# Kernel tuning notes

Measured on AMD Instinct MI355X. Metric: run time of the kernel, lower is better.

Reference implementation:

```python
import jax, jax.numpy as jnp
import numpy as np

# Static config (from set_param of the wrapped deformable conv)
N, CIN, H, W = 8, 64, 128, 128
COUT, KH, KW = 64, 3, 3
STRIDE, PAD, DIL = 1, 1, 1
WEIGHT_BIT = 8
K = KH * KW
HO = (H + 2 * PAD - DIL * (KH - 1) - 1) // STRIDE + 1
WO = (W + 2 * PAD - DIL * (KW - 1) - 1) // STRIDE + 1


def setup_inputs() -> dict:
    key = jax.random.key(0)
    k1, k2, k3 = jax.random.split(key, 3)
    x = jax.random.normal(k1, (N, CIN, H, W), dtype=jnp.float32)
    offset = jax.random.normal(k2, (N, 2 * K, HO, WO), dtype=jnp.float32)
    weight = jax.random.normal(k3, (COUT, CIN, KH, KW), dtype=jnp.float32) * 0.05
    return {"x": x, "offset": offset, "weight": weight}


def quantize_weight_symmetric(w, bits):
    # HAWQ/CoDeNet symmetric per-tensor quant: scale = max(|min|,|max|)/n,
    # q = clamp(round(w/scale), -n-1, n) * scale, straight-through estimator.
    n = 2 ** (bits - 1) - 1
    sat = jnp.maximum(jnp.abs(w.min()), jnp.abs(w.max()))
    scale = jnp.maximum(sat, 1e-8) / n
    wq = jnp.clip(jnp.round(w / scale), -n - 1, n) * scale
    return w + jax.lax.stop_gradient(wq - w)


def deform_conv2d(x, offset, weight):
    # x: [N,C,H,W]; offset: [N, 2*K, HO, WO] (y,x interleaved per kernel tap)
    # Base sampling grid for each kernel tap and output location.
    ky, kx = jnp.meshgrid(jnp.arange(KH), jnp.arange(KW), indexing='ij')
    ky = ky.reshape(K).astype(jnp.float32)  # [K]
    kx = kx.reshape(K).astype(jnp.float32)
    ho = jnp.arange(HO, dtype=jnp.float32)
    wo = jnp.arange(WO, dtype=jnp.float32)
    base_y = ho[None, :, None] * STRIDE - PAD + ky[:, None, None] * DIL  # [K,HO,1]
    base_x = wo[None, None, :] * STRIDE - PAD + kx[:, None, None] * DIL  # [K,1,WO]

    off = offset.reshape(N, K, 2, HO, WO)
    py = base_y[None] + off[:, :, 0]  # [N,K,HO,WO]
    px = base_x[None] + off[:, :, 1]

    y0 = jnp.floor(py)
    x0 = jnp.floor(px)
    dy = py - y0
    dx = px - x0
    y0i = y0.astype(jnp.int32)
    x0i = x0.astype(jnp.int32)

    xf = x.reshape(N, CIN, H * W)

    def gather_corner(yi, xi, wgt):
        # zero padding outside the image
        valid = (yi >= 0) & (yi < H) & (xi >= 0) & (xi < W)
        idx = jnp.clip(yi, 0, H - 1) * W + jnp.clip(xi, 0, W - 1)  # [N,K,HO,WO]
        vals = jax.vmap(lambda xn, idn: xn[:, idn.reshape(-1)])(xf, idx)
        vals = vals.reshape(N, CIN, K, HO, WO)
        return vals * (wgt * valid.astype(wgt.dtype))[:, None]  # [N,1,K,HO,WO]

    sampled = (
        gather_corner(y0i, x0i, (1.0 - dy) * (1.0 - dx))
        + gather_corner(y0i, x0i + 1, (1.0 - dy) * dx)
        + gather_corner(y0i + 1, x0i, dy * (1.0 - dx))
        + gather_corner(y0i + 1, x0i + 1, dy * dx)
    )  # [N,CIN,K,HO,WO]

    out = jnp.einsum('nckhw,ock->nohw', sampled, weight.reshape(COUT, CIN, K))
    return out


def reference(x, offset, weight):
    wq = quantize_weight_symmetric(weight, WEIGHT_BIT)
    return deform_conv2d(x, offset, wq)
```

## Files before the change

### kernel.cpp

```cpp
#include <hip/hip_runtime.h>
#include <hip/hip_bf16.h>

#define NB    8
#define CCH   64
#define HH    128
#define WW    128
#define KTAP  9
#define HW    (HH * WW)
#define KSTEPS 18
#define NW    36864

typedef _Float16 f16x8 __attribute__((ext_vector_type(8)));
typedef _Float16 f16x2 __attribute__((ext_vector_type(2)));
typedef __attribute__((ext_vector_type(4))) float f32x4;

__device__ inline unsigned int pack_f16(float a, float b) {
    f16x2 h;
    h[0] = (_Float16)a;
    h[1] = (_Float16)b;
    return __builtin_bit_cast(unsigned int, h);
}

__device__ inline f16x8 as_f16x8(uint4 u) { return __builtin_bit_cast(f16x8, u); }

__global__ __launch_bounds__(256) void prep_kernel(const float* __restrict__ x,
                                                   const float* __restrict__ w,
                                                   unsigned int* __restrict__ xt32,
                                                   uint4* __restrict__ bq) {
    __shared__ float tile[64 * 65];
    const int t = threadIdx.x;
    const int bid = blockIdx.x;

    if (bid < 2048) {
        const int n = bid >> 8;
        const int pbase = (bid & 255) * 64;
        #pragma unroll
        for (int i = 0; i < 4; i++) {
            int idx = i * 256 + t;
            int c = idx >> 4, f4 = idx & 15;
            float4 v = *(const float4*)&x[((size_t)(n * CCH + c)) * HW + pbase + f4 * 4];
            float* d = &tile[c * 65 + f4 * 4];
            d[0] = v.x; d[1] = v.y; d[2] = v.z; d[3] = v.w;
        }
        __syncthreads();
        const int px = t >> 2, c4 = t & 3;
        float f[16];
        #pragma unroll
        for (int j = 0; j < 16; j++) f[j] = tile[(c4 * 16 + j) * 65 + px];
        unsigned int o8[8];
        #pragma unroll
        for (int i = 0; i < 8; i++) o8[i] = pack_f16(f[2 * i], f[2 * i + 1]);
        uint4* dst = (uint4*)&xt32[((size_t)(n * HW + pbase + px)) * 32 + c4 * 8];
        dst[0] = make_uint4(o8[0], o8[1], o8[2], o8[3]);
        dst[1] = make_uint4(o8[4], o8[5], o8[6], o8[7]);
    } else {
        float m0 = 0.f, m1 = 0.f, m2 = 0.f, m3 = 0.f;
        for (int i = t; i < NW; i += 1024) {
            m0 = fmaxf(m0, fabsf(w[i]));
            m1 = fmaxf(m1, fabsf(w[i + 256]));
            m2 = fmaxf(m2, fabsf(w[i + 512]));
            m3 = fmaxf(m3, fabsf(w[i + 768]));
        }
        float m = fmaxf(fmaxf(m0, m1), fmaxf(m2, m3));
        #pragma unroll
        for (int off = 32; off > 0; off >>= 1)
            m = fmaxf(m, __shfl_down(m, off));
        if ((t & 63) == 0) tile[t >> 6] = m;
        __syncthreads();
        m = fmaxf(fmaxf(tile[0], tile[1]), fmaxf(tile[2], tile[3]));
        const float scale = fmaxf(m, 1e-8f) / 127.f;
        const float inv_scale = 1.f / scale;

        const int rec = (bid - 2048) * 256 + t;
        int nt  = rec / (KSTEPS * 64);
        int rem = rec - nt * (KSTEPS * 64);
        int s    = rem >> 6;
        int lane = rem & 63;
        int quad = lane >> 4, n16 = lane & 15;
        int o = nt * 16 + n16;
        unsigned int u[4];
        #pragma unroll
        for (int jj = 0; jj < 4; jj++) {
            float q[2];
            #pragma unroll
            for (int h = 0; h < 2; h++) {
                int k   = s * 32 + quad * 8 + 2 * jj + h;
                int c   = k & 63;
                int tap = k >> 6;
                float v  = w[(o * CCH + c) * KTAP + tap];
                float qq = rintf(v * inv_scale);
                q[h] = fminf(fmaxf(qq, -128.f), 127.f) * scale;
            }
            u[jj] = pack_f16(q[0], q[1]);
        }
        bq[rec] = make_uint4(u[0], u[1], u[2], u[3]);
    }
}

__global__ __launch_bounds__(256) void deform_mfma(const unsigned short* __restrict__ xt,
                                                   const float* __restrict__ offset,
                                                   const uint4* __restrict__ bq,
                                                   float* __restrict__ out) {
    __shared__ unsigned int SC[576];
    __shared__ uint2 SW[576];
    __shared__ _Float16 Abuf[2][64 * 64];

    const int t    = threadIdx.x;
    const int wid  = t >> 6;
    const int lane = t & 63;
    const int quad = lane >> 4, n16 = lane & 15;
    const int bid  = blockIdx.x;
    const int n    = bid & 7;
    const int px0  = (bid >> 3) * 64;
    const int pl   = t >> 2;
    const int c4   = t & 3;

    const char* xb = (const char*)(xt + (size_t)n * HW * CCH);
    const float* offn = offset + (size_t)n * 2 * KTAP * HW;
    const uint4* bqw = bq + (size_t)wid * KSTEPS * 64 + lane;

    for (int u = t; u < 576; u += 256) {
        const int tap = u >> 6, p = u & 63;
        const int ppx = px0 + p;
        const int ho = ppx >> 7, wo = ppx & 127;
        const int ky = tap / 3, kx = tap - 3 * ky;
        const float py  = (float)(ho - 1 + ky) + offn[(2 * tap) * HW + ppx];
        const float pxf = (float)(wo - 1 + kx) + offn[(2 * tap + 1) * HW + ppx];
        const float fy = floorf(py), fx = floorf(pxf);
        const int y0 = (int)fy, x0 = (int)fx;
        const float dy = py - fy, dx = pxf - fx;
        const int y1 = y0 + 1, x1 = x0 + 1;
        const bool vy0 = (y0 >= 0) && (y0 < HH);
        const bool vy1 = (y1 >= 0) && (y1 < HH);
        const bool vx0 = (x0 >= 0) && (x0 < WW);
        const bool vx1 = (x1 >= 0) && (x1 < WW);
        const int y0c = min(max(y0, 0), HH - 1);
        const int y1c = min(max(y1, 0), HH - 1);
        const int x0c = min(max(x0, 0), WW - 1);
        const int x1c = min(max(x1, 0), WW - 1);
        const float w00 = (1.f - dy) * (1.f - dx) * ((vy0 && vx0) ? 1.f : 0.f);
        const float w01 = (1.f - dy) * dx         * ((vy0 && vx1) ? 1.f : 0.f);
        const float w10 = dy * (1.f - dx)         * ((vy1 && vx0) ? 1.f : 0.f);
        const float w11 = dy * dx                 * ((vy1 && vx1) ? 1.f : 0.f);
        SC[u] = (unsigned)(y0c | (x0c << 7) | (y1c << 14) | (x1c << 21));
        SW[u] = make_uint2(pack_f16(w00, w01), pack_f16(w10, w11));
    }

    f32x4 acc[4];
    #pragma unroll
    for (int mt = 0; mt < 4; mt++) acc[mt] = (f32x4){0.f, 0.f, 0.f, 0.f};

    const int cb = c4 * 16;
    const int p7 = pl & 7;

    uint4 rbuf[2][8];
    uint4 bbuf[2][2];

    auto issue = [&](int tap, int b) {
        bbuf[b][0] = bqw[(tap * 2 + 0) * 64];
        bbuf[b][1] = bqw[(tap * 2 + 1) * 64];
        const unsigned int cc = SC[tap * 64 + pl];
        const int y0b = (int)(cc & 127) << 14;
        const int x0b = (int)((cc >> 7) & 127) << 7;
        const int y1b = (int)((cc >> 14) & 127) << 14;
        const int x1b = (int)(cc >> 21) << 7;
        const char* q00 = xb + (y0b | x0b) + cb;
        const char* q01 = xb + (y0b | x1b) + cb;
        const char* q10 = xb + (y1b | x0b) + cb;
        const char* q11 = xb + (y1b | x1b) + cb;
        rbuf[b][0] = *(const uint4*)q00; rbuf[b][1] = *(const uint4*)(q00 + 64);
        rbuf[b][2] = *(const uint4*)q01; rbuf[b][3] = *(const uint4*)(q01 + 64);
        rbuf[b][4] = *(const uint4*)q10; rbuf[b][5] = *(const uint4*)(q10 + 64);
        rbuf[b][6] = *(const uint4*)q11; rbuf[b][7] = *(const uint4*)(q11 + 64);
    };

    auto blend = [&](int tap, int b) {
        const uint2 ww = SW[tap * 64 + pl];
        const f16x2 wA = __builtin_bit_cast(f16x2, ww.x);
        const f16x2 wB = __builtin_bit_cast(f16x2, ww.y);
        f16x8 sa = as_f16x8(rbuf[b][0]) * wA[0];
        sa += as_f16x8(rbuf[b][2]) * wA[1];
        sa += as_f16x8(rbuf[b][4]) * wB[0];
        sa += as_f16x8(rbuf[b][6]) * wB[1];
        f16x8 sb = as_f16x8(rbuf[b][1]) * wA[0];
        sb += as_f16x8(rbuf[b][3]) * wA[1];
        sb += as_f16x8(rbuf[b][5]) * wB[0];
        sb += as_f16x8(rbuf[b][7]) * wB[1];
        *(f16x8*)&Abuf[b][pl * 64 + ((c4 ^ p7) * 8)]       = sa;
        *(f16x8*)&Abuf[b][pl * 64 + (((4 + c4) ^ p7) * 8)] = sb;
    };

    auto mma_tap = [&](int tap, int b) {
        #pragma unroll
        for (int sl = 0; sl < 2; sl++) {
            const f16x8 bf = __builtin_bit_cast(f16x8, bbuf[b][sl]);
            #pragma unroll
            for (int mt = 0; mt < 4; mt++) {
                const int rr = mt * 16 + n16;
                const int slot = (sl * 4 + quad) ^ (n16 & 7);
                const f16x8 a = *(const f16x8*)&Abuf[b][rr * 64 + slot * 8];
                acc[mt] = __builtin_amdgcn_mfma_f32_16x16x32_f16(a, bf, acc[mt], 0, 0, 0);
            }
        }
    };

    __syncthreads();
    issue(0, 0);
    #pragma unroll
    for (int tap = 0; tap < KTAP; tap++) {
        if (tap < KTAP - 1) issue(tap + 1, (tap + 1) & 1);
        blend(tap, tap & 1);
        __syncthreads();
        mma_tap(tap, tap & 1);
    }

    const int o = wid * 16 + n16;
    #pragma unroll
    for (int mt = 0; mt < 4; mt++) {
        float4 v = make_float4(acc[mt].x, acc[mt].y, acc[mt].z, acc[mt].w);
        float* dst = out + ((size_t)(n * CCH + o)) * HW + px0 + mt * 16 + quad * 4;
        *(float4*)dst = v;
    }
}

extern "C" void kernel_launch(void* const* d_in, const int* in_sizes, int n_in,
                              void* d_out, int out_size, void* d_ws, size_t ws_size,
                              hipStream_t stream) {
    const float* x      = (const float*)d_in[0];
    const float* offset = (const float*)d_in[1];
    const float* weight = (const float*)d_in[2];
    float* out = (float*)d_out;

    unsigned char* ws = (unsigned char*)d_ws;
    uint4*        bq   = (uint4*)ws;
    unsigned int* xt32 = (unsigned int*)(ws + 131072);
    const unsigned short* xt = (const unsigned short*)xt32;

    prep_kernel<<<2048 + 18, 256, 0, stream>>>(x, weight, xt32, bq);
    deform_mfma<<<2048, 256, 0, stream>>>(xt, offset, bq, out);
}
```

Before: 132.2 us.

## Feed blended samples straight into MFMA registers, dropping LDS staging and double buffering

Each wave now owns 16 pixels and computes the bilinear blend directly in the MFMA A-operand register layout, then loops over all four output-channel tiles. This removes the shared-memory A buffer, its write/read traffic and the per-tap block barriers. In exchange it drops the software prefetch of the next tap (the loop is now unroll 1), and each wave reloads the full weight set for all channel tiles, which raises global/L2 weight traffic and may expose gather latency.

```diff
diff --git a/kernel.cpp b/kernel.cpp
--- a/kernel.cpp
+++ b/kernel.cpp
@@ -103,7 +103,6 @@
                                                    float* __restrict__ out) {
     __shared__ unsigned int SC[576];
     __shared__ uint2 SW[576];
-    __shared__ _Float16 Abuf[2][64 * 64];
 
     const int t    = threadIdx.x;
     const int wid  = t >> 6;
@@ -112,12 +111,10 @@
     const int bid  = blockIdx.x;
     const int n    = bid & 7;
     const int px0  = (bid >> 3) * 64;
-    const int pl   = t >> 2;
-    const int c4   = t & 3;
+    const int mypix = wid * 16 + n16;
 
     const char* xb = (const char*)(xt + (size_t)n * HW * CCH);
     const float* offn = offset + (size_t)n * 2 * KTAP * HW;
-    const uint4* bqw = bq + (size_t)wid * KSTEPS * 64 + lane;
 
     for (int u = t; u < 576; u += 256) {
         const int tap = u >> 6, p = u & 63;
@@ -145,21 +142,17 @@
         SC[u] = (unsigned)(y0c | (x0c << 7) | (y1c << 14) | (x1c << 21));
         SW[u] = make_uint2(pack_f16(w00, w01), pack_f16(w10, w11));
     }
+    __syncthreads();
 
     f32x4 acc[4];
     #pragma unroll
-    for (int mt = 0; mt < 4; mt++) acc[mt] = (f32x4){0.f, 0.f, 0.f, 0.f};
-
-    const int cb = c4 * 16;
-    const int p7 = pl & 7;
-
-    uint4 rbuf[2][8];
-    uint4 bbuf[2][2];
-
-    auto issue = [&](int tap, int b) {
-        bbuf[b][0] = bqw[(tap * 2 + 0) * 64];
-        bbuf[b][1] = bqw[(tap * 2 + 1) * 64];
-        const unsigned int cc = SC[tap * 64 + pl];
+    for (int nt = 0; nt < 4; nt++) acc[nt] = (f32x4){0.f, 0.f, 0.f, 0.f};
+
+    const int cb = quad * 16;
+
+    #pragma unroll 1
+    for (int tap = 0; tap < KTAP; tap++) {
+        const unsigned int cc = SC[tap * 64 + mypix];
         const int y0b = (int)(cc & 127) << 14;
         const int x0b = (int)((cc >> 7) & 127) << 7;
         const int y1b = (int)((cc >> 14) & 127) << 14;
@@ -168,57 +161,44 @@
         const char* q01 = xb + (y0b | x1b) + cb;
         const char* q10 = xb + (y1b | x0b) + cb;
         const char* q11 = xb + (y1b | x1b) + cb;
-        rbuf[b][0] = *(const uint4*)q00; rbuf[b][1] = *(const uint4*)(q00 + 64);
-        rbuf[b][2] = *(const uint4*)q01; rbuf[b][3] = *(const uint4*)(q01 + 64);
-        rbuf[b][4] = *(const uint4*)q10; rbuf[b][5] = *(const uint4*)(q10 + 64);
-        rbuf[b][6] = *(const uint4*)q11; rbuf[b][7] = *(const uint4*)(q11 + 64);
-    };
-
-    auto blend = [&](int tap, int b) {
-        const uint2 ww = SW[tap * 64 + pl];
+        uint4 r0 = *(const uint4*)q00, r1 = *(const uint4*)(q00 + 64);
+        uint4 r2 = *(const uint4*)q01, r3 = *(const uint4*)(q01 + 64);
+        uint4 r4 = *(const uint4*)q10, r5 = *(const uint4*)(q10 + 64);
+        uint4 r6 = *(const uint4*)q11, r7 = *(const uint4*)(q11 + 64);
+
+        uint4 bf[8];
+        #pragma unroll
+        for (int nt = 0; nt < 4; nt++) {
+            bf[nt * 2 + 0] = bq[((nt * KSTEPS) + tap * 2 + 0) * 64 + lane];
+            bf[nt * 2 + 1] = bq[((nt * KSTEPS) + tap * 2 + 1) * 64 + lane];
+        }
+
+        const uint2 ww = SW[tap * 64 + mypix];
         const f16x2 wA = __builtin_bit_cast(f16x2, ww.x);
         const f16x2 wB = __builtin_bit_cast(f16x2, ww.y);
-        f16x8 sa = as_f16x8(rbuf[b][0]) * wA[0];
-        sa += as_f16x8(rbuf[b][2]) * wA[1];
-        sa += as_f16x8(rbuf[b][4]) * wB[0];
-        sa += as_f16x8(rbuf[b][6]) * wB[1];
-        f16x8 sb = as_f16x8(rbuf[b][1]) * wA[0];
-        sb += as_f16x8(rbuf[b][3]) * wA[1];
-        sb += as_f16x8(rbuf[b][5]) * wB[0];
-        sb += as_f16x8(rbuf[b][7]) * wB[1];
-        *(f16x8*)&Abuf[b][pl * 64 + ((c4 ^ p7) * 8)]       = sa;
-        *(f16x8*)&Abuf[b][pl * 64 + (((4 + c4) ^ p7) * 8)] = sb;
-    };
-
-    auto mma_tap = [&](int tap, int b) {
-        #pragma unroll
-        for (int sl = 0; sl < 2; sl++) {
-            const f16x8 bf = __builtin_bit_cast(f16x8, bbuf[b][sl]);
-            #pragma unroll
-            for (int mt = 0; mt < 4; mt++) {
-                const int rr = mt * 16 + n16;
-                const int slot = (sl * 4 + quad) ^ (n16 & 7);
-                const f16x8 a = *(const f16x8*)&Abuf[b][rr * 64 + slot * 8];
-                acc[mt] = __builtin_amdgcn_mfma_f32_16x16x32_f16(a, bf, acc[mt], 0, 0, 0);
-            }
-        }
-    };
-
-    __syncthreads();
-    issue(0, 0);
+        f16x8 sa = as_f16x8(r0) * wA[0];
+        sa += as_f16x8(r2) * wA[1];
+        sa += as_f16x8(r4) * wB[0];
+        sa += as_f16x8(r6) * wB[1];
+        f16x8 sb = as_f16x8(r1) * wA[0];
+        sb += as_f16x8(r3) * wA[1];
+        sb += as_f16x8(r5) * wB[0];
+        sb += as_f16x8(r7) * wB[1];
+
+        #pragma unroll
+        for (int nt = 0; nt < 4; nt++) {
+            acc[nt] = __builtin_amdgcn_mfma_f32_16x16x32_f16(
+                sa, __builtin_bit_cast(f16x8, bf[nt * 2 + 0]), acc[nt], 0, 0, 0);
+            acc[nt] = __builtin_amdgcn_mfma_f32_16x16x32_f16(
+                sb, __builtin_bit_cast(f16x8, bf[nt * 2 + 1]), acc[nt], 0, 0, 0);
+        }
+    }
+
     #pragma unroll
-    for (int tap = 0; tap < KTAP; tap++) {
-        if (tap < KTAP - 1) issue(tap + 1, (tap + 1) & 1);
-        blend(tap, tap & 1);
-        __syncthreads();
-        mma_tap(tap, tap & 1);
-    }
-
-    const int o = wid * 16 + n16;
-    #pragma unroll
-    for (int mt = 0; mt < 4; mt++) {
-        float4 v = make_float4(acc[mt].x, acc[mt].y, acc[mt].z, acc[mt].w);
-        float* dst = out + ((size_t)(n * CCH + o)) * HW + px0 + mt * 16 + quad * 4;
+    for (int nt = 0; nt < 4; nt++) {
+        const int o = nt * 16 + n16;
+        float4 v = make_float4(acc[nt].x, acc[nt].y, acc[nt].z, acc[nt].w);
+        float* dst = out + ((size_t)(n * CCH + o)) * HW + px0 + wid * 16 + quad * 4;
         *(float4*)dst = v;
     }
 }
```

New measurement: 179.5 us. 35.8% more time.

## Process two taps per pipeline stage to halve block barriers

Applied to the files above, without the earlier changes.

Restructures the main loop so each stage gathers, blends and multiplies two kernel taps at once, cutting the stage count from nine to five and the number of __syncthreads barriers accordingly. The shared A buffer grows to hold two taps per stage, doubling LDS use. Gathers for the next stage are now issued after the current blend instead of before it, so less gather latency is hidden behind the blend. The larger per-stage register set may lower occupancy.

```diff
diff --git a/kernel.cpp b/kernel.cpp
--- a/kernel.cpp
+++ b/kernel.cpp
@@ -101,9 +101,9 @@
                                                    const float* __restrict__ offset,
                                                    const uint4* __restrict__ bq,
                                                    float* __restrict__ out) {
+    __shared__ _Float16 Abuf[2][2][4096];
     __shared__ unsigned int SC[576];
     __shared__ uint2 SW[576];
-    __shared__ _Float16 Abuf[2][64 * 64];
 
     const int t    = threadIdx.x;
     const int wid  = t >> 6;
@@ -114,10 +114,11 @@
     const int px0  = (bid >> 3) * 64;
     const int pl   = t >> 2;
     const int c4   = t & 3;
+    const int cb   = c4 * 16;
+    const int p7   = pl & 7;
 
     const char* xb = (const char*)(xt + (size_t)n * HW * CCH);
     const float* offn = offset + (size_t)n * 2 * KTAP * HW;
-    const uint4* bqw = bq + (size_t)wid * KSTEPS * 64 + lane;
 
     for (int u = t; u < 576; u += 256) {
         const int tap = u >> 6, p = u & 63;
@@ -145,20 +146,16 @@
         SC[u] = (unsigned)(y0c | (x0c << 7) | (y1c << 14) | (x1c << 21));
         SW[u] = make_uint2(pack_f16(w00, w01), pack_f16(w10, w11));
     }
+    __syncthreads();
 
     f32x4 acc[4];
     #pragma unroll
     for (int mt = 0; mt < 4; mt++) acc[mt] = (f32x4){0.f, 0.f, 0.f, 0.f};
 
-    const int cb = c4 * 16;
-    const int p7 = pl & 7;
-
-    uint4 rbuf[2][8];
-    uint4 bbuf[2][2];
-
-    auto issue = [&](int tap, int b) {
-        bbuf[b][0] = bqw[(tap * 2 + 0) * 64];
-        bbuf[b][1] = bqw[(tap * 2 + 1) * 64];
+    uint4 rset[16];
+    uint4 bset[2][4];
+
+    auto gather8 = [&](int tap, uint4* r) {
         const unsigned int cc = SC[tap * 64 + pl];
         const int y0b = (int)(cc & 127) << 14;
         const int x0b = (int)((cc >> 7) & 127) << 7;
@@ -168,50 +165,59 @@
         const char* q01 = xb + (y0b | x1b) + cb;
         const char* q10 = xb + (y1b | x0b) + cb;
         const char* q11 = xb + (y1b | x1b) + cb;
-        rbuf[b][0] = *(const uint4*)q00; rbuf[b][1] = *(const uint4*)(q00 + 64);
-        rbuf[b][2] = *(const uint4*)q01; rbuf[b][3] = *(const uint4*)(q01 + 64);
-        rbuf[b][4] = *(const uint4*)q10; rbuf[b][5] = *(const uint4*)(q10 + 64);
-        rbuf[b][6] = *(const uint4*)q11; rbuf[b][7] = *(const uint4*)(q11 + 64);
-    };
-
-    auto blend = [&](int tap, int b) {
+        r[0] = *(const uint4*)q00; r[1] = *(const uint4*)(q00 + 64);
+        r[2] = *(const uint4*)q01; r[3] = *(const uint4*)(q01 + 64);
+        r[4] = *(const uint4*)q10; r[5] = *(const uint4*)(q10 + 64);
+        r[6] = *(const uint4*)q11; r[7] = *(const uint4*)(q11 + 64);
+    };
+    auto issue_stage = [&](int s) {
+        gather8(2 * s, rset);
+        if (s < 4) gather8(2 * s + 1, rset + 8);
+        const int nk = (s < 4) ? 4 : 2;
+        for (int k = 0; k < nk; k++)
+            bset[s & 1][k] = bq[((size_t)wid * KSTEPS + 4 * s + k) * 64 + lane];
+    };
+    auto blend1 = [&](int tap, const uint4* r, _Float16* sub) {
         const uint2 ww = SW[tap * 64 + pl];
         const f16x2 wA = __builtin_bit_cast(f16x2, ww.x);
         const f16x2 wB = __builtin_bit_cast(f16x2, ww.y);
-        f16x8 sa = as_f16x8(rbuf[b][0]) * wA[0];
-        sa += as_f16x8(rbuf[b][2]) * wA[1];
-        sa += as_f16x8(rbuf[b][4]) * wB[0];
-        sa += as_f16x8(rbuf[b][6]) * wB[1];
-        f16x8 sb = as_f16x8(rbuf[b][1]) * wA[0];
-        sb += as_f16x8(rbuf[b][3]) * wA[1];
-        sb += as_f16x8(rbuf[b][5]) * wB[0];
-        sb += as_f16x8(rbuf[b][7]) * wB[1];
-        *(f16x8*)&Abuf[b][pl * 64 + ((c4 ^ p7) * 8)]       = sa;
-        *(f16x8*)&Abuf[b][pl * 64 + (((4 + c4) ^ p7) * 8)] = sb;
-    };
-
-    auto mma_tap = [&](int tap, int b) {
-        #pragma unroll
-        for (int sl = 0; sl < 2; sl++) {
-            const f16x8 bf = __builtin_bit_cast(f16x8, bbuf[b][sl]);
+        f16x8 sa = as_f16x8(r[0]) * wA[0];
+        sa += as_f16x8(r[2]) * wA[1];
+        sa += as_f16x8(r[4]) * wB[0];
+        sa += as_f16x8(r[6]) * wB[1];
+        f16x8 sb = as_f16x8(r[1]) * wA[0];
+        sb += as_f16x8(r[3]) * wA[1];
+        sb += as_f16x8(r[5]) * wB[0];
+        sb += as_f16x8(r[7]) * wB[1];
+        *(f16x8*)&sub[pl * 64 + ((c4 ^ p7) * 8)]       = sa;
+        *(f16x8*)&sub[pl * 64 + (((4 + c4) ^ p7) * 8)] = sb;
+    };
+    auto blend_stage = [&](int s) {
+        blend1(2 * s, rset, Abuf[s & 1][0]);
+        if (s < 4) blend1(2 * s + 1, rset + 8, Abuf[s & 1][1]);
+    };
+    auto mma_stage = [&](int s) {
+        const int nk = (s < 4) ? 4 : 2;
+        for (int ks = 0; ks < nk; ks++) {
+            const _Float16* sub = Abuf[s & 1][ks >> 1];
+            const f16x8 bf = __builtin_bit_cast(f16x8, bset[s & 1][ks]);
             #pragma unroll
             for (int mt = 0; mt < 4; mt++) {
                 const int rr = mt * 16 + n16;
-                const int slot = (sl * 4 + quad) ^ (n16 & 7);
-                const f16x8 a = *(const f16x8*)&Abuf[b][rr * 64 + slot * 8];
+                const int slot = ((ks & 1) * 4 + quad) ^ (n16 & 7);
+                const f16x8 a = *(const f16x8*)&sub[rr * 64 + slot * 8];
                 acc[mt] = __builtin_amdgcn_mfma_f32_16x16x32_f16(a, bf, acc[mt], 0, 0, 0);
             }
         }
     };
 
-    __syncthreads();
-    issue(0, 0);
+    issue_stage(0);
     #pragma unroll
-    for (int tap = 0; tap < KTAP; tap++) {
-        if (tap < KTAP - 1) issue(tap + 1, (tap + 1) & 1);
-        blend(tap, tap & 1);
+    for (int s = 0; s < 5; s++) {
+        blend_stage(s);
+        if (s < 4) issue_stage(s + 1);
         __syncthreads();
-        mma_tap(tap, tap & 1);
+        mma_stage(s);
     }
 
     const int o = wid * 16 + n16;
```

New measurement: 131.1 us. Within noise of the previous version (-0.8%).
